# Performance work log

Measured on AMD Instinct MI355X. Metric: run time of the kernel, lower is better.

## Reference

```python
import jax, jax.numpy as jnp
import numpy as np

DIM, HEADS, DEPTH, SEQ, LOCAL_W = 1024, 16, 7, 2048, 64
HEAD_DIM = DIM // HEADS
SCALE = 1.0 / HEAD_DIM ** 0.5


def cantor_mask(S, depth, local_window):
    """Allowed (i,j): |i-j| within local window, OR |i-j| lies in the Cantor set
    under `depth` levels of ternary subdivision (no base-3 digit equals 1)."""
    idx = np.arange(S)
    d = np.abs(idx[:, None] - idx[None, :])
    x = d.copy()
    ok = np.ones_like(d, dtype=bool)
    for _ in range(depth):
        ok &= (x % 3) != 1
        x //= 3
    ok &= x == 0  # offset must be < 3**depth
    return jnp.asarray(ok | (d <= local_window))  # [S, S] bool


def setup_inputs() -> dict:
    key = jax.random.key(0)
    ks = jax.random.split(key, 8)
    B = 2
    s = 0.02
    return {
        "query": jax.random.normal(ks[0], (B, SEQ, DIM), jnp.float32),
        "key_value": jax.random.normal(ks[1], (B, SEQ, DIM), jnp.float32),
        "Wq": jax.random.normal(ks[2], (DIM, DIM), jnp.float32) * s,
        "bq": jnp.zeros((DIM,), jnp.float32),
        "Wkv": jax.random.normal(ks[3], (DIM, 2 * DIM), jnp.float32) * s,
        "bkv": jnp.zeros((2 * DIM,), jnp.float32),
        "Wo": jax.random.normal(ks[4], (DIM, DIM), jnp.float32) * s,
        "bo": jnp.zeros((DIM,), jnp.float32),
    }


def reference(query, key_value, Wq, bq, Wkv, bkv, Wo, bo):
    B, S, D = query.shape
    H, hd = HEADS, HEAD_DIM
    mask = cantor_mask(S, DEPTH, LOCAL_W)  # static [S, S] bool

    q = (query @ Wq + bq).reshape(B, S, H, hd).transpose(0, 2, 1, 3)  # [B,H,S,hd]
    kv = (key_value @ Wkv + bkv).reshape(B, S, 2, H, hd).transpose(2, 0, 3, 1, 4)
    k, v = kv[0], kv[1]  # [B,H,S,hd]

    scores = jnp.einsum("bhqd,bhkd->bhqk", q, k) * SCALE
    scores = jnp.where(mask, scores, jnp.finfo(scores.dtype).min)
    attn = jax.nn.softmax(scores, axis=-1)
    out = jnp.einsum("bhqk,bhkd->bhqd", attn, v)  # [B,H,S,hd]
    out = out.transpose(0, 2, 1, 3).reshape(B, S, D)
    return out @ Wo + bo
```

## Files before the change

### kernel.cpp

```cpp
#include <hip/hip_runtime.h>
#include <stdint.h>

typedef _Float16 half_t;
typedef __attribute__((ext_vector_type(8))) _Float16 half8;
typedef __attribute__((ext_vector_type(4))) _Float16 half4;
typedef __attribute__((ext_vector_type(4))) float floatx4;

#define SEQ 2048
#define NH 16
#define HD 64

#define MFMA16(a, b, c) __builtin_amdgcn_mfma_f32_16x16x16f16(a, b, c, 0, 0, 0)

#define QSCALE 0.1803368801111306f

__global__ __launch_bounds__(256) void init_all(uint8_t* __restrict__ tok,
                                                uint64_t* __restrict__ maskw) {
  __shared__ uint8_t slut[2048];
  int t = threadIdx.x;
  for (int d = t; d < 2048; d += 256) {
    int x = d;
    bool ok = true;
    for (int it = 0; it < 7; ++it) { ok &= ((x % 3) != 1); x /= 3; }
    ok &= (x == 0);
    slut[d] = (ok || d <= 64) ? 1 : 0;
  }
  __syncthreads();
  if (blockIdx.x == 0 && t < 64) {
    int delta = t - 32;
    int lo = delta * 64 - 63, hi = delta * 64 + 63;
    uint8_t any = 0;
    for (int x = lo; x <= hi; ++x) {
      int a = x < 0 ? -x : x;
      if (a < 2048) any |= slut[a];
    }
    tok[t] = any;
  }
  int g = blockIdx.x * 256 + t;
  int tt = g - 2048;
  uint64_t w = 0;
  for (int jj = 0; jj < 64; ++jj) {
    int d = tt - jj; d = d < 0 ? -d : d;
    if (d < 2048 && slut[d]) w |= (1ull << jj);
  }
  maskw[g] = w;
}

__global__ __launch_bounds__(256) void cast_f2h2(const float* __restrict__ a,
                                                 const float* __restrict__ b,
                                                 half_t* __restrict__ da,
                                                 half_t* __restrict__ db) {
  int bx = blockIdx.x;
  const float* s;
  half_t* d;
  int i;
  if (bx < 4096) { s = a; d = da; i = (bx * 256 + threadIdx.x) * 4; }
  else { s = b; d = db; i = ((bx - 4096) * 256 + threadIdx.x) * 4; }
  floatx4 v = *(const floatx4*)(s + i);
  half4 h;
  h[0] = (half_t)v[0]; h[1] = (half_t)v[1];
  h[2] = (half_t)v[2]; h[3] = (half_t)v[3];
  *(half4*)(d + i) = h;
}

__global__ __launch_bounds__(256) void transpose_cast3(
    const float* __restrict__ Wq, const float* __restrict__ Wkv,
    const float* __restrict__ Wo, half_t* __restrict__ wqT,
    half_t* __restrict__ wkvT, half_t* __restrict__ woT) {
  __shared__ float tile[32][33];
  int z = blockIdx.z;
  const float* W = (z == 0) ? Wq : ((z == 1) ? Wkv : Wo);
  half_t* Wt = (z == 0) ? wqT : ((z == 1) ? wkvT : woT);
  int N = (z == 1) ? 2048 : 1024;
  const int K = 1024;
  int n0 = blockIdx.x * 32, k0 = blockIdx.y * 32;
  if (n0 >= N) return;
  int tx = threadIdx.x & 31, ty = threadIdx.x >> 5;
#pragma unroll
  for (int i = 0; i < 4; ++i)
    tile[ty + i * 8][tx] = W[(size_t)(k0 + ty + i * 8) * N + n0 + tx];
  __syncthreads();
#pragma unroll
  for (int i = 0; i < 4; ++i)
    Wt[(size_t)(n0 + ty + i * 8) * K + k0 + tx] = (half_t)tile[tx][ty + i * 8];
}

__device__ __forceinline__ void cp16(half_t* lds, const half_t* g) {
  __builtin_amdgcn_global_load_lds(
      (const __attribute__((address_space(1))) uint32_t*)g,
      (__attribute__((address_space(3))) uint32_t*)lds, 16, 0, 0);
}

__global__ __launch_bounds__(256) void gemm_qkv(
    const half_t* __restrict__ xq, const half_t* __restrict__ xkv,
    const half_t* __restrict__ wqT, const half_t* __restrict__ wkvT,
    const float* __restrict__ bq, const float* __restrict__ bkv,
    half_t* __restrict__ qout, half_t* __restrict__ kout,
    half_t* __restrict__ vToutg) {
  __shared__ half_t As[2][128 * 32];
  __shared__ half_t Bs[2][128 * 32];
  const int K = 1024;
  bool isq = blockIdx.y < 8;
  const half_t* A = isq ? xq : xkv;
  const half_t* Bt = isq ? wqT : wkvT;
  const float* bias = isq ? bq : bkv;
  int n0 = (isq ? blockIdx.y : (blockIdx.y - 8)) * 128;
  int m0 = blockIdx.x * 128;

  int tid = threadIdx.x;
  int wave = tid >> 6, lane = tid & 63;
  int c = lane & 15, quad = lane >> 4;
  int wm = (wave >> 1) * 64, wn = (wave & 1) * 64;

  floatx4 acc[4][4] = {};
  int arow = tid >> 2, akc = (tid & 3) * 8;

  cp16(&As[0][wave * 512], A + (size_t)(m0 + arow) * K + akc);
  cp16(&As[0][2048 + wave * 512], A + (size_t)(m0 + 64 + arow) * K + akc);
  cp16(&Bs[0][wave * 512], Bt + (size_t)(n0 + arow) * K + akc);
  cp16(&Bs[0][2048 + wave * 512], Bt + (size_t)(n0 + 64 + arow) * K + akc);

  for (int kt = 0; kt < 32; ++kt) {
    __syncthreads();
    if (kt + 1 < 32) {
      int k0 = (kt + 1) * 32;
      int b = (kt + 1) & 1;
      cp16(&As[b][wave * 512], A + (size_t)(m0 + arow) * K + k0 + akc);
      cp16(&As[b][2048 + wave * 512], A + (size_t)(m0 + 64 + arow) * K + k0 + akc);
      cp16(&Bs[b][wave * 512], Bt + (size_t)(n0 + arow) * K + k0 + akc);
      cp16(&Bs[b][2048 + wave * 512], Bt + (size_t)(n0 + 64 + arow) * K + k0 + akc);
    }
    int b = kt & 1;
    half8 af[4], bf[4];
#pragma unroll
    for (int mt = 0; mt < 4; ++mt)
      af[mt] = *(const half8*)&As[b][(wm + mt * 16 + c) * 32 + quad * 8];
#pragma unroll
    for (int nt = 0; nt < 4; ++nt)
      bf[nt] = *(const half8*)&Bs[b][(wn + nt * 16 + c) * 32 + quad * 8];
#pragma unroll
    for (int mt = 0; mt < 4; ++mt)
#pragma unroll
      for (int nt = 0; nt < 4; ++nt)
        acc[mt][nt] = __builtin_amdgcn_mfma_f32_16x16x32_f16(af[mt], bf[nt],
                                                             acc[mt][nt], 0, 0, 0);
  }

#pragma unroll
  for (int nt = 0; nt < 4; ++nt) {
    int n = n0 + wn + nt * 16 + c;
    float bv = bias[n];
    bool isv = !isq && (n >> 10);
    int h = (n >> 6) & 15, d = n & 63;
#pragma unroll
    for (int mt = 0; mt < 4; ++mt) {
      int mbase = m0 + wm + mt * 16 + quad * 4;
      int bb = mbase >> 11, s = mbase & 2047;
      if (isv) {
        half4 hv;
#pragma unroll
        for (int r = 0; r < 4; ++r) hv[r] = (half_t)(acc[mt][nt][r] + bv);
        *(half4*)(vToutg + ((size_t)(bb * 16 + h) * 64 + d) * SEQ + s) = hv;
      } else if (isq) {
#pragma unroll
        for (int r = 0; r < 4; ++r)
          qout[(((size_t)(bb * 16 + h) * SEQ + s + r) * 64) + d] =
              (half_t)((acc[mt][nt][r] + bv) * QSCALE);
      } else {
#pragma unroll
        for (int r = 0; r < 4; ++r)
          kout[(((size_t)(bb * 16 + h) * SEQ + s + r) * 64) + d] =
              (half_t)(acc[mt][nt][r] + bv);
      }
    }
  }
}

__global__ __launch_bounds__(256) void gemm_out(
    const half_t* __restrict__ A, const half_t* __restrict__ Bt,
    const float* __restrict__ bias, float* __restrict__ outf) {
  __shared__ half_t As[2][128 * 32];
  __shared__ half_t Bs[2][64 * 32];
  const int K = 1024;
  int tid = threadIdx.x;
  int wave = tid >> 6, lane = tid & 63;
  int c = lane & 15, quad = lane >> 4;
  int wm = (wave >> 1) * 64, wn = (wave & 1) * 32;
  int m0 = blockIdx.x * 128, n0 = blockIdx.y * 64;

  floatx4 acc[4][2] = {};
  int arow = tid >> 2, akc = (tid & 3) * 8;

  cp16(&As[0][wave * 512], A + (size_t)(m0 + arow) * K + akc);
  cp16(&As[0][2048 + wave * 512], A + (size_t)(m0 + 64 + arow) * K + akc);
  cp16(&Bs[0][wave * 512], Bt + (size_t)(n0 + arow) * K + akc);

  for (int kt = 0; kt < 32; ++kt) {
    __syncthreads();
    if (kt + 1 < 32) {
      int k0 = (kt + 1) * 32;
      int b = (kt + 1) & 1;
      cp16(&As[b][wave * 512], A + (size_t)(m0 + arow) * K + k0 + akc);
      cp16(&As[b][2048 + wave * 512], A + (size_t)(m0 + 64 + arow) * K + k0 + akc);
      cp16(&Bs[b][wave * 512], Bt + (size_t)(n0 + arow) * K + k0 + akc);
    }
    int b = kt & 1;
    half8 af[4], bf[2];
#pragma unroll
    for (int mt = 0; mt < 4; ++mt)
      af[mt] = *(const half8*)&As[b][(wm + mt * 16 + c) * 32 + quad * 8];
#pragma unroll
    for (int nt = 0; nt < 2; ++nt)
      bf[nt] = *(const half8*)&Bs[b][(wn + nt * 16 + c) * 32 + quad * 8];
#pragma unroll
    for (int mt = 0; mt < 4; ++mt)
#pragma unroll
      for (int nt = 0; nt < 2; ++nt)
        acc[mt][nt] = __builtin_amdgcn_mfma_f32_16x16x32_f16(af[mt], bf[nt],
                                                             acc[mt][nt], 0, 0, 0);
  }

#pragma unroll
  for (int nt = 0; nt < 2; ++nt) {
    int n = n0 + wn + nt * 16 + c;
    float bv = bias[n];
#pragma unroll
    for (int mt = 0; mt < 4; ++mt)
#pragma unroll
      for (int r = 0; r < 4; ++r) {
        int m = m0 + wm + mt * 16 + quad * 4 + r;
        outf[(size_t)m * 1024 + n] = acc[mt][nt][r] + bv;
      }
  }
}

__global__ __launch_bounds__(256) void attn_kernel(
    const half_t* __restrict__ qb, const half_t* __restrict__ kb,
    const half_t* __restrict__ vTg, half_t* __restrict__ ctx,
    const uint64_t* __restrict__ maskw, const uint8_t* __restrict__ tok) {
  __shared__ half_t kT[64 * 64];
  __shared__ half_t vT[64 * 64];
  __shared__ half_t ot[64 * 72];
  __shared__ int list[34];

  int tid = threadIdx.x, wave = tid >> 6, lane = tid & 63;
  int c = lane & 15, q = lane >> 4;
  int i0 = blockIdx.x * 64;
  int bh = blockIdx.y;
  const half_t* qbase = qb + (size_t)bh * SEQ * HD;
  const half_t* kg = kb + (size_t)bh * SEQ * HD;
  const half_t* vg = vTg + (size_t)bh * HD * SEQ;

  if (wave == 0) {
    int jt = lane;
    bool act = (jt < 32) && tok[(jt - (i0 >> 6)) + 32];
    unsigned long long bal = __ballot(act);
    if (act) {
      int pre = __popcll(bal & ((1ull << jt) - 1));
      list[1 + pre] = jt << 6;
    }
    if (lane == 0) list[0] = __popcll(bal);
  }

  int i_row = i0 + wave * 16 + c;
  half8 qf0 = *(const half8*)(qbase + (size_t)i_row * 64 + q * 8);
  half8 qf1 = *(const half8*)(qbase + (size_t)i_row * 64 + 32 + q * 8);

  floatx4 oacc[4] = {};
  floatx4 lacc = {};
  half4 ones;
  ones[0] = (half_t)1.f; ones[1] = (half_t)1.f;
  ones[2] = (half_t)1.f; ones[3] = (half_t)1.f;

  int srow = tid >> 2;
  int sch = (tid & 3) * 2;
  int ssw = srow & 7;

  __syncthreads();
  int nact = list[0];
  int j0 = list[1];

  half8 kr0 = *(const half8*)(kg + (size_t)(j0 + srow) * 64 + sch * 8);
  half8 kr1 = *(const half8*)(kg + (size_t)(j0 + srow) * 64 + sch * 8 + 8);
  half8 vr0 = *(const half8*)(vg + (size_t)srow * SEQ + j0 + sch * 8);
  half8 vr1 = *(const half8*)(vg + (size_t)srow * SEQ + j0 + sch * 8 + 8);

  for (int ti = 0; ti < nact; ++ti) {
    uint64_t w = maskw[(i_row - j0) + 2048];
    __syncthreads();
    *(half8*)&kT[srow * 64 + ((sch ^ ssw) * 8)] = kr0;
    *(half8*)&kT[srow * 64 + (((sch + 1) ^ ssw) * 8)] = kr1;
    *(half8*)&vT[srow * 64 + ((sch ^ ssw) * 8)] = vr0;
    *(half8*)&vT[srow * 64 + (((sch + 1) ^ ssw) * 8)] = vr1;
    int j0n = j0;
    if (ti + 1 < nact) {
      j0n = list[2 + ti];
      kr0 = *(const half8*)(kg + (size_t)(j0n + srow) * 64 + sch * 8);
      kr1 = *(const half8*)(kg + (size_t)(j0n + srow) * 64 + sch * 8 + 8);
      vr0 = *(const half8*)(vg + (size_t)srow * SEQ + j0n + sch * 8);
      vr1 = *(const half8*)(vg + (size_t)srow * SEQ + j0n + sch * 8 + 8);
    }
    __syncthreads();

    floatx4 sc[4];
#pragma unroll
    for (int jt = 0; jt < 4; ++jt) {
      int row = jt * 16 + c;
      int sw = row & 7;
      half8 a0 = *(const half8*)&kT[row * 64 + ((q ^ sw) * 8)];
      half8 a1 = *(const half8*)&kT[row * 64 + (((4 + q) ^ sw) * 8)];
      floatx4 t = {};
      t = __builtin_amdgcn_mfma_f32_16x16x32_f16(a0, qf0, t, 0, 0, 0);
      t = __builtin_amdgcn_mfma_f32_16x16x32_f16(a1, qf1, t, 0, 0, 0);
      sc[jt] = t;
    }

    uint32_t wlo = (uint32_t)(w >> (4 * q));
    uint32_t whi = (uint32_t)(w >> (32 + 4 * q));
    half4 pb[4];
#pragma unroll
    for (int jt = 0; jt < 4; ++jt) {
      uint32_t ww = (jt < 2) ? wlo : whi;
#pragma unroll
      for (int r = 0; r < 4; ++r) {
        float p = __builtin_exp2f(sc[jt][r]);
        int bitpos = 16 * (jt & 1) + r;
        uint32_t msk = (uint32_t)(((int)(ww << (31 - bitpos))) >> 31);
        sc[jt][r] = __uint_as_float(__float_as_uint(p) & msk);
      }
      auto lo = __builtin_amdgcn_cvt_pkrtz(sc[jt][0], sc[jt][1]);
      auto hi = __builtin_amdgcn_cvt_pkrtz(sc[jt][2], sc[jt][3]);
      half4 pbv; pbv[0] = lo[0]; pbv[1] = lo[1]; pbv[2] = hi[0]; pbv[3] = hi[1];
      pb[jt] = pbv;
    }

#pragma unroll
    for (int jt = 0; jt < 4; ++jt) lacc = MFMA16(ones, pb[jt], lacc);

#pragma unroll
    for (int mt = 0; mt < 4; ++mt) {
      int drow = mt * 16 + c;
      int sw = drow & 7;
      floatx4 o = oacc[mt];
#pragma unroll
      for (int jt = 0; jt < 4; ++jt) {
        int ch = 2 * jt + (q >> 1);
        half4 a = *(const half4*)&vT[drow * 64 + ((ch ^ sw) * 8) + (q & 1) * 4];
        o = MFMA16(a, pb[jt], o);
      }
      oacc[mt] = o;
    }
    j0 = j0n;
  }

  float inv_l = 1.0f / lacc[0];
#pragma unroll
  for (int mt = 0; mt < 4; ++mt)
#pragma unroll
    for (int r = 0; r < 4; ++r)
      ot[(wave * 16 + c) * 72 + mt * 16 + 4 * q + r] = (half_t)(oacc[mt][r] * inv_l);
  __syncthreads();
  {
    int row = tid >> 2, chq = tid & 3;
    int b = bh >> 4, h = bh & 15;
    size_t base = (((size_t)(b * SEQ + i0 + row) * NH) + h) * 64 + chq * 16;
    half8 v0 = *(const half8*)&ot[row * 72 + chq * 16];
    half8 v1 = *(const half8*)&ot[row * 72 + chq * 16 + 8];
    *(half8*)(ctx + base) = v0;
    *(half8*)(ctx + base + 8) = v1;
  }
}

extern "C" void kernel_launch(void* const* d_in, const int* in_sizes, int n_in,
                              void* d_out, int out_size, void* d_ws, size_t ws_size,
                              hipStream_t stream) {
  const float* query = (const float*)d_in[0];
  const float* key_value = (const float*)d_in[1];
  const float* Wq = (const float*)d_in[2];
  const float* bq = (const float*)d_in[3];
  const float* Wkv = (const float*)d_in[4];
  const float* bkv = (const float*)d_in[5];
  const float* Wo = (const float*)d_in[6];
  const float* bo = (const float*)d_in[7];

  char* ws = (char*)d_ws;
  uint8_t* tok = (uint8_t*)ws;
  uint64_t* maskw = (uint64_t*)(ws + 4096);
  const size_t MB = 1ull << 20;
  half_t* xq = (half_t*)(ws + 1 * MB);
  half_t* xkv = (half_t*)(ws + 9 * MB);
  half_t* wqT = (half_t*)(ws + 17 * MB);
  half_t* wkvT = (half_t*)(ws + 19 * MB);
  half_t* woT = (half_t*)(ws + 23 * MB);
  half_t* qbuf = (half_t*)(ws + 25 * MB);
  half_t* kbuf = (half_t*)(ws + 33 * MB);
  half_t* vTg = (half_t*)(ws + 41 * MB);
  half_t* ctx = xq;

  hipLaunchKernelGGL(init_all, dim3(16), dim3(256), 0, stream, tok, maskw);
  hipLaunchKernelGGL(cast_f2h2, dim3(8192), dim3(256), 0, stream,
                     query, key_value, xq, xkv);
  hipLaunchKernelGGL(transpose_cast3, dim3(64, 32, 3), dim3(256), 0, stream,
                     Wq, Wkv, Wo, wqT, wkvT, woT);
  hipLaunchKernelGGL(gemm_qkv, dim3(32, 24), dim3(256), 0, stream,
                     xq, xkv, wqT, wkvT, bq, bkv, qbuf, kbuf, vTg);
  hipLaunchKernelGGL(attn_kernel, dim3(32, 32), dim3(256), 0, stream,
                     qbuf, kbuf, vTg, ctx, maskw, tok);
  hipLaunchKernelGGL(gemm_out, dim3(32, 16), dim3(256), 0, stream,
                     ctx, woT, bo, (float*)d_out);
}
```

Measured before the change: 226.8 us.

## Merge prep kernels, stage QKV epilogue through LDS, skip empty 16-key subtiles

```diff
diff --git a/kernel.cpp b/kernel.cpp
--- a/kernel.cpp
+++ b/kernel.cpp
@@ -11,14 +11,52 @@
 #define HD 64
 
 #define MFMA16(a, b, c) __builtin_amdgcn_mfma_f32_16x16x16f16(a, b, c, 0, 0, 0)
+#define MFMA32K(a, b, c) __builtin_amdgcn_mfma_f32_16x16x32_f16(a, b, c, 0, 0, 0)
 
 #define QSCALE 0.1803368801111306f
 
-__global__ __launch_bounds__(256) void init_all(uint8_t* __restrict__ tok,
-                                                uint64_t* __restrict__ maskw) {
+__global__ __launch_bounds__(256) void prep(
+    const float* __restrict__ query, const float* __restrict__ key_value,
+    const float* __restrict__ Wq, const float* __restrict__ Wkv,
+    const float* __restrict__ Wo, half_t* __restrict__ xq,
+    half_t* __restrict__ xkv, half_t* __restrict__ wqT,
+    half_t* __restrict__ wkvT, half_t* __restrict__ woT,
+    uint8_t* __restrict__ tok, uint8_t* __restrict__ tok16,
+    uint64_t* __restrict__ maskw) {
+  int bx = blockIdx.x, tid = threadIdx.x;
+  if (bx < 8192) {
+    const float* s; half_t* d; int i;
+    if (bx < 4096) { s = query; d = xq; i = (bx * 256 + tid) * 4; }
+    else { s = key_value; d = xkv; i = ((bx - 4096) * 256 + tid) * 4; }
+    floatx4 v = *(const floatx4*)(s + i);
+    half4 h;
+    h[0] = (half_t)v[0]; h[1] = (half_t)v[1];
+    h[2] = (half_t)v[2]; h[3] = (half_t)v[3];
+    *(half4*)(d + i) = h;
+    return;
+  }
+  if (bx < 12288) {
+    __shared__ float tile[32][33];
+    int id = bx - 8192;
+    const float* W; half_t* Wt; int N, nt, kt;
+    if (id < 1024) { W = Wq; Wt = wqT; N = 1024; nt = id & 31; kt = id >> 5; }
+    else if (id < 3072) { int i2 = id - 1024; W = Wkv; Wt = wkvT; N = 2048; nt = i2 & 63; kt = i2 >> 6; }
+    else { int i2 = id - 3072; W = Wo; Wt = woT; N = 1024; nt = i2 & 31; kt = i2 >> 5; }
+    const int K = 1024;
+    int n0 = nt * 32, k0 = kt * 32;
+    int tx = tid & 31, ty = tid >> 5;
+#pragma unroll
+    for (int i = 0; i < 4; ++i)
+      tile[ty + i * 8][tx] = W[(size_t)(k0 + ty + i * 8) * N + n0 + tx];
+    __syncthreads();
+#pragma unroll
+    for (int i = 0; i < 4; ++i)
+      Wt[(size_t)(n0 + ty + i * 8) * K + k0 + tx] = (half_t)tile[tx][ty + i * 8];
+    return;
+  }
   __shared__ uint8_t slut[2048];
-  int t = threadIdx.x;
-  for (int d = t; d < 2048; d += 256) {
+  int ib = bx - 12288;
+  for (int d = tid; d < 2048; d += 256) {
     int x = d;
     bool ok = true;
     for (int it = 0; it < 7; ++it) { ok &= ((x % 3) != 1); x /= 3; }
@@ -26,17 +64,29 @@
     slut[d] = (ok || d <= 64) ? 1 : 0;
   }
   __syncthreads();
-  if (blockIdx.x == 0 && t < 64) {
-    int delta = t - 32;
-    int lo = delta * 64 - 63, hi = delta * 64 + 63;
-    uint8_t any = 0;
-    for (int x = lo; x <= hi; ++x) {
-      int a = x < 0 ? -x : x;
-      if (a < 2048) any |= slut[a];
-    }
-    tok[t] = any;
-  }
-  int g = blockIdx.x * 256 + t;
+  if (ib == 0) {
+    if (tid < 64) {
+      int delta = tid - 32;
+      int lo = delta * 64 - 63, hi = delta * 64 + 63;
+      uint8_t any = 0;
+      for (int x = lo; x <= hi; ++x) {
+        int a = x < 0 ? -x : x;
+        if (a < 2048) any |= slut[a];
+      }
+      tok[tid] = any;
+    }
+    {
+      int d16 = tid - 128;
+      int ctr = d16 * 16;
+      uint8_t any = 0;
+      for (int x = ctr - 15; x <= ctr + 15; ++x) {
+        int a = x < 0 ? -x : x;
+        if (a < 2048) any |= slut[a];
+      }
+      tok16[tid] = any;
+    }
+  }
+  int g = ib * 256 + tid;
   int tt = g - 2048;
   uint64_t w = 0;
   for (int jj = 0; jj < 64; ++jj) {
@@ -46,45 +96,6 @@
   maskw[g] = w;
 }
 
-__global__ __launch_bounds__(256) void cast_f2h2(const float* __restrict__ a,
-                                                 const float* __restrict__ b,
-                                                 half_t* __restrict__ da,
-                                                 half_t* __restrict__ db) {
-  int bx = blockIdx.x;
-  const float* s;
-  half_t* d;
-  int i;
-  if (bx < 4096) { s = a; d = da; i = (bx * 256 + threadIdx.x) * 4; }
-  else { s = b; d = db; i = ((bx - 4096) * 256 + threadIdx.x) * 4; }
-  floatx4 v = *(const floatx4*)(s + i);
-  half4 h;
-  h[0] = (half_t)v[0]; h[1] = (half_t)v[1];
-  h[2] = (half_t)v[2]; h[3] = (half_t)v[3];
-  *(half4*)(d + i) = h;
-}
-
-__global__ __launch_bounds__(256) void transpose_cast3(
-    const float* __restrict__ Wq, const float* __restrict__ Wkv,
-    const float* __restrict__ Wo, half_t* __restrict__ wqT,
-    half_t* __restrict__ wkvT, half_t* __restrict__ woT) {
-  __shared__ float tile[32][33];
-  int z = blockIdx.z;
-  const float* W = (z == 0) ? Wq : ((z == 1) ? Wkv : Wo);
-  half_t* Wt = (z == 0) ? wqT : ((z == 1) ? wkvT : woT);
-  int N = (z == 1) ? 2048 : 1024;
-  const int K = 1024;
-  int n0 = blockIdx.x * 32, k0 = blockIdx.y * 32;
-  if (n0 >= N) return;
-  int tx = threadIdx.x & 31, ty = threadIdx.x >> 5;
-#pragma unroll
-  for (int i = 0; i < 4; ++i)
-    tile[ty + i * 8][tx] = W[(size_t)(k0 + ty + i * 8) * N + n0 + tx];
-  __syncthreads();
-#pragma unroll
-  for (int i = 0; i < 4; ++i)
-    Wt[(size_t)(n0 + ty + i * 8) * K + k0 + tx] = (half_t)tile[tx][ty + i * 8];
-}
-
 __device__ __forceinline__ void cp16(half_t* lds, const half_t* g) {
   __builtin_amdgcn_global_load_lds(
       (const __attribute__((address_space(1))) uint32_t*)g,
@@ -96,9 +107,10 @@
     const half_t* __restrict__ wqT, const half_t* __restrict__ wkvT,
     const float* __restrict__ bq, const float* __restrict__ bkv,
     half_t* __restrict__ qout, half_t* __restrict__ kout,
-    half_t* __restrict__ vToutg) {
-  __shared__ half_t As[2][128 * 32];
-  __shared__ half_t Bs[2][128 * 32];
+    half_t* __restrict__ vTout) {
+  extern __shared__ char smemraw[];
+  half_t* As = (half_t*)smemraw;
+  half_t* Bs = As + 8192;
   const int K = 1024;
   bool isq = blockIdx.y < 8;
   const half_t* A = isq ? xq : xkv;
@@ -115,63 +127,90 @@
   floatx4 acc[4][4] = {};
   int arow = tid >> 2, akc = (tid & 3) * 8;
 
-  cp16(&As[0][wave * 512], A + (size_t)(m0 + arow) * K + akc);
-  cp16(&As[0][2048 + wave * 512], A + (size_t)(m0 + 64 + arow) * K + akc);
-  cp16(&Bs[0][wave * 512], Bt + (size_t)(n0 + arow) * K + akc);
-  cp16(&Bs[0][2048 + wave * 512], Bt + (size_t)(n0 + 64 + arow) * K + akc);
+  cp16(&As[wave * 512], A + (size_t)(m0 + arow) * K + akc);
+  cp16(&As[2048 + wave * 512], A + (size_t)(m0 + 64 + arow) * K + akc);
+  cp16(&Bs[wave * 512], Bt + (size_t)(n0 + arow) * K + akc);
+  cp16(&Bs[2048 + wave * 512], Bt + (size_t)(n0 + 64 + arow) * K + akc);
 
   for (int kt = 0; kt < 32; ++kt) {
     __syncthreads();
     if (kt + 1 < 32) {
       int k0 = (kt + 1) * 32;
       int b = (kt + 1) & 1;
-      cp16(&As[b][wave * 512], A + (size_t)(m0 + arow) * K + k0 + akc);
-      cp16(&As[b][2048 + wave * 512], A + (size_t)(m0 + 64 + arow) * K + k0 + akc);
-      cp16(&Bs[b][wave * 512], Bt + (size_t)(n0 + arow) * K + k0 + akc);
-      cp16(&Bs[b][2048 + wave * 512], Bt + (size_t)(n0 + 64 + arow) * K + k0 + akc);
+      cp16(&As[b * 4096 + wave * 512], A + (size_t)(m0 + arow) * K + k0 + akc);
+      cp16(&As[b * 4096 + 2048 + wave * 512], A + (size_t)(m0 + 64 + arow) * K + k0 + akc);
+      cp16(&Bs[b * 4096 + wave * 512], Bt + (size_t)(n0 + arow) * K + k0 + akc);
+      cp16(&Bs[b * 4096 + 2048 + wave * 512], Bt + (size_t)(n0 + 64 + arow) * K + k0 + akc);
     }
     int b = kt & 1;
     half8 af[4], bf[4];
 #pragma unroll
     for (int mt = 0; mt < 4; ++mt)
-      af[mt] = *(const half8*)&As[b][(wm + mt * 16 + c) * 32 + quad * 8];
+      af[mt] = *(const half8*)&As[b * 4096 + (wm + mt * 16 + c) * 32 + quad * 8];
 #pragma unroll
     for (int nt = 0; nt < 4; ++nt)
-      bf[nt] = *(const half8*)&Bs[b][(wn + nt * 16 + c) * 32 + quad * 8];
+      bf[nt] = *(const half8*)&Bs[b * 4096 + (wn + nt * 16 + c) * 32 + quad * 8];
 #pragma unroll
     for (int mt = 0; mt < 4; ++mt)
 #pragma unroll
       for (int nt = 0; nt < 4; ++nt)
-        acc[mt][nt] = __builtin_amdgcn_mfma_f32_16x16x32_f16(af[mt], bf[nt],
-                                                             acc[mt][nt], 0, 0, 0);
-  }
-
-#pragma unroll
-  for (int nt = 0; nt < 4; ++nt) {
-    int n = n0 + wn + nt * 16 + c;
-    float bv = bias[n];
-    bool isv = !isq && (n >> 10);
-    int h = (n >> 6) & 15, d = n & 63;
-#pragma unroll
-    for (int mt = 0; mt < 4; ++mt) {
-      int mbase = m0 + wm + mt * 16 + quad * 4;
-      int bb = mbase >> 11, s = mbase & 2047;
-      if (isv) {
+        acc[mt][nt] = MFMA32K(af[mt], bf[nt], acc[mt][nt]);
+  }
+
+  __syncthreads();
+  half_t* ep = (half_t*)smemraw;
+  int bb = m0 >> 11, sbase = m0 & 2047;
+  bool isv = (!isq) && (n0 >= 1024);
+
+  if (!isv) {
+#pragma unroll
+    for (int nt = 0; nt < 4; ++nt) {
+      int nl = wn + nt * 16 + c;
+      float bv = bias[n0 + nl];
+#pragma unroll
+      for (int mt = 0; mt < 4; ++mt)
+#pragma unroll
+        for (int r = 0; r < 4; ++r) {
+          int ml = wm + mt * 16 + quad * 4 + r;
+          float v = acc[mt][nt][r] + bv;
+          if (isq) v *= QSCALE;
+          ep[ml * 128 + nl] = (half_t)v;
+        }
+    }
+    __syncthreads();
+    half_t* outp = isq ? qout : kout;
+#pragma unroll
+    for (int rd = 0; rd < 8; ++rd) {
+      int id = rd * 256 + tid;
+      int ml = id >> 4, ch = id & 15;
+      int ng = n0 + ch * 8;
+      int h = ng >> 6, d0 = ng & 63;
+      half8 v = *(const half8*)&ep[ml * 128 + ch * 8];
+      *(half8*)(outp + ((size_t)(bb * 16 + h) * SEQ + sbase + ml) * 64 + d0) = v;
+    }
+  } else {
+#pragma unroll
+    for (int nt = 0; nt < 4; ++nt) {
+      int nl = wn + nt * 16 + c;
+      float bv = bias[n0 + nl];
+#pragma unroll
+      for (int mt = 0; mt < 4; ++mt) {
+        int ml = wm + mt * 16 + quad * 4;
         half4 hv;
 #pragma unroll
         for (int r = 0; r < 4; ++r) hv[r] = (half_t)(acc[mt][nt][r] + bv);
-        *(half4*)(vToutg + ((size_t)(bb * 16 + h) * 64 + d) * SEQ + s) = hv;
-      } else if (isq) {
-#pragma unroll
-        for (int r = 0; r < 4; ++r)
-          qout[(((size_t)(bb * 16 + h) * SEQ + s + r) * 64) + d] =
-              (half_t)((acc[mt][nt][r] + bv) * QSCALE);
-      } else {
-#pragma unroll
-        for (int r = 0; r < 4; ++r)
-          kout[(((size_t)(bb * 16 + h) * SEQ + s + r) * 64) + d] =
-              (half_t)(acc[mt][nt][r] + bv);
-      }
+        *(half4*)&ep[nl * 136 + ml] = hv;
+      }
+    }
+    __syncthreads();
+#pragma unroll
+    for (int rd = 0; rd < 8; ++rd) {
+      int id = rd * 256 + tid;
+      int nl = id >> 4, mc = id & 15;
+      int ng = n0 + nl;
+      int h = (ng >> 6) & 15, d = ng & 63;
+      half8 v = *(const half8*)&ep[nl * 136 + mc * 8];
+      *(half8*)(vTout + ((size_t)(bb * 16 + h) * 64 + d) * SEQ + sbase + mc * 8) = v;
     }
   }
 }
@@ -216,8 +255,7 @@
     for (int mt = 0; mt < 4; ++mt)
 #pragma unroll
       for (int nt = 0; nt < 2; ++nt)
-        acc[mt][nt] = __builtin_amdgcn_mfma_f32_16x16x32_f16(af[mt], bf[nt],
-                                                             acc[mt][nt], 0, 0, 0);
+        acc[mt][nt] = MFMA32K(af[mt], bf[nt], acc[mt][nt]);
   }
 
 #pragma unroll
@@ -237,11 +275,13 @@
 __global__ __launch_bounds__(256) void attn_kernel(
     const half_t* __restrict__ qb, const half_t* __restrict__ kb,
     const half_t* __restrict__ vTg, half_t* __restrict__ ctx,
-    const uint64_t* __restrict__ maskw, const uint8_t* __restrict__ tok) {
+    const uint64_t* __restrict__ maskw, const uint8_t* __restrict__ tok,
+    const uint8_t* __restrict__ tok16g) {
   __shared__ half_t kT[64 * 64];
   __shared__ half_t vT[64 * 64];
   __shared__ half_t ot[64 * 72];
   __shared__ int list[34];
+  __shared__ uint8_t tok16s[256];
 
   int tid = threadIdx.x, wave = tid >> 6, lane = tid & 63;
   int c = lane & 15, q = lane >> 4;
@@ -251,6 +291,7 @@
   const half_t* kg = kb + (size_t)bh * SEQ * HD;
   const half_t* vg = vTg + (size_t)bh * HD * SEQ;
 
+  tok16s[tid] = tok16g[tid];
   if (wave == 0) {
     int jt = lane;
     bool act = (jt < 32) && tok[(jt - (i0 >> 6)) + 32];
@@ -263,6 +304,7 @@
   }
 
   int i_row = i0 + wave * 16 + c;
+  int it16 = (i0 >> 4) + wave;
   half8 qf0 = *(const half8*)(qbase + (size_t)i_row * 64 + q * 8);
   half8 qf1 = *(const half8*)(qbase + (size_t)i_row * 64 + 32 + q * 8);
 
@@ -287,6 +329,7 @@
 
   for (int ti = 0; ti < nact; ++ti) {
     uint64_t w = maskw[(i_row - j0) + 2048];
+    int bidx = (j0 >> 4) - it16 + 128;
     __syncthreads();
     *(half8*)&kT[srow * 64 + ((sch ^ ssw) * 8)] = kr0;
     *(half8*)&kT[srow * 64 + (((sch + 1) ^ ssw) * 8)] = kr1;
@@ -302,53 +345,38 @@
     }
     __syncthreads();
 
-    floatx4 sc[4];
+    uint32_t wlo = (uint32_t)(w >> (4 * q));
+    uint32_t whi = (uint32_t)(w >> (32 + 4 * q));
 #pragma unroll
     for (int jt = 0; jt < 4; ++jt) {
+      if (!tok16s[bidx + jt]) continue;
       int row = jt * 16 + c;
-      int sw = row & 7;
+      int sw = c & 7;
       half8 a0 = *(const half8*)&kT[row * 64 + ((q ^ sw) * 8)];
       half8 a1 = *(const half8*)&kT[row * 64 + (((4 + q) ^ sw) * 8)];
       floatx4 t = {};
-      t = __builtin_amdgcn_mfma_f32_16x16x32_f16(a0, qf0, t, 0, 0, 0);
-      t = __builtin_amdgcn_mfma_f32_16x16x32_f16(a1, qf1, t, 0, 0, 0);
-      sc[jt] = t;
-    }
-
-    uint32_t wlo = (uint32_t)(w >> (4 * q));
-    uint32_t whi = (uint32_t)(w >> (32 + 4 * q));
-    half4 pb[4];
-#pragma unroll
-    for (int jt = 0; jt < 4; ++jt) {
+      t = MFMA32K(a0, qf0, t);
+      t = MFMA32K(a1, qf1, t);
       uint32_t ww = (jt < 2) ? wlo : whi;
 #pragma unroll
       for (int r = 0; r < 4; ++r) {
-        float p = __builtin_exp2f(sc[jt][r]);
+        float p = __builtin_exp2f(t[r]);
         int bitpos = 16 * (jt & 1) + r;
         uint32_t msk = (uint32_t)(((int)(ww << (31 - bitpos))) >> 31);
-        sc[jt][r] = __uint_as_float(__float_as_uint(p) & msk);
-      }
-      auto lo = __builtin_amdgcn_cvt_pkrtz(sc[jt][0], sc[jt][1]);
-      auto hi = __builtin_amdgcn_cvt_pkrtz(sc[jt][2], sc[jt][3]);
-      half4 pbv; pbv[0] = lo[0]; pbv[1] = lo[1]; pbv[2] = hi[0]; pbv[3] = hi[1];
-      pb[jt] = pbv;
-    }
-
-#pragma unroll
-    for (int jt = 0; jt < 4; ++jt) lacc = MFMA16(ones, pb[jt], lacc);
-
-#pragma unroll
-    for (int mt = 0; mt < 4; ++mt) {
-      int drow = mt * 16 + c;
-      int sw = drow & 7;
-      floatx4 o = oacc[mt];
-#pragma unroll
-      for (int jt = 0; jt < 4; ++jt) {
+        t[r] = __uint_as_float(__float_as_uint(p) & msk);
+      }
+      auto lo = __builtin_amdgcn_cvt_pkrtz(t[0], t[1]);
+      auto hi = __builtin_amdgcn_cvt_pkrtz(t[2], t[3]);
+      half4 pb;
+      pb[0] = lo[0]; pb[1] = lo[1]; pb[2] = hi[0]; pb[3] = hi[1];
+      lacc = MFMA16(ones, pb, lacc);
+#pragma unroll
+      for (int mt = 0; mt < 4; ++mt) {
+        int drow = mt * 16 + c;
         int ch = 2 * jt + (q >> 1);
         half4 a = *(const half4*)&vT[drow * 64 + ((ch ^ sw) * 8) + (q & 1) * 4];
-        o = MFMA16(a, pb[jt], o);
-      }
-      oacc[mt] = o;
+        oacc[mt] = MFMA16(a, pb, oacc[mt]);
+      }
     }
     j0 = j0n;
   }
@@ -385,6 +413,7 @@
 
   char* ws = (char*)d_ws;
   uint8_t* tok = (uint8_t*)ws;
+  uint8_t* tok16 = (uint8_t*)(ws + 1024);
   uint64_t* maskw = (uint64_t*)(ws + 4096);
   const size_t MB = 1ull << 20;
   half_t* xq = (half_t*)(ws + 1 * MB);
@@ -397,15 +426,13 @@
   half_t* vTg = (half_t*)(ws + 41 * MB);
   half_t* ctx = xq;
 
-  hipLaunchKernelGGL(init_all, dim3(16), dim3(256), 0, stream, tok, maskw);
-  hipLaunchKernelGGL(cast_f2h2, dim3(8192), dim3(256), 0, stream,
-                     query, key_value, xq, xkv);
-  hipLaunchKernelGGL(transpose_cast3, dim3(64, 32, 3), dim3(256), 0, stream,
-                     Wq, Wkv, Wo, wqT, wkvT, woT);
-  hipLaunchKernelGGL(gemm_qkv, dim3(32, 24), dim3(256), 0, stream,
+  hipLaunchKernelGGL(prep, dim3(12304), dim3(256), 0, stream,
+                     query, key_value, Wq, Wkv, Wo, xq, xkv, wqT, wkvT, woT,
+                     tok, tok16, maskw);
+  hipLaunchKernelGGL(gemm_qkv, dim3(32, 24), dim3(256), 34816, stream,
                      xq, xkv, wqT, wkvT, bq, bkv, qbuf, kbuf, vTg);
   hipLaunchKernelGGL(attn_kernel, dim3(32, 32), dim3(256), 0, stream,
-                     qbuf, kbuf, vTg, ctx, maskw, tok);
+                     qbuf, kbuf, vTg, ctx, maskw, tok, tok16);
   hipLaunchKernelGGL(gemm_out, dim3(32, 16), dim3(256), 0, stream,
                      ctx, woT, bo, (float*)d_out);
 }
```

New measurement: 226.3 us. About the same (-0.2%).
